# Performance work log

Hardware: AMD Instinct MI355X
Metric: run time of the kernel (lower is better)

The kernel has to match this reference:

```python
import jax, jax.numpy as jnp
import numpy as np

DIM = 512
H = 8
HD = 64          # hidden_dim = dim // num_heads
TD = 64          # time_dim -> time features = 2*TD = 128
LIN = 1536
EPS = 1e-5

def layer_norm(x, g, b):
    mu = jnp.mean(x, axis=-1, keepdims=True)
    var = jnp.mean((x - mu) ** 2, axis=-1, keepdims=True)
    return (x - mu) * jax.lax.rsqrt(var + EPS) * g + b

def setup_inputs() -> dict:
    key = jax.random.key(0)
    ks = jax.random.split(key, 16)
    B, L = 2, 2048
    return {
        "tensor": jax.random.normal(ks[0], (B, L, DIM), jnp.float32),
        "attention_mask": jnp.ones((B, L), jnp.float32),
        "time_angle": jax.random.uniform(ks[1], (H, TD), jnp.float32),
        "head_time_delta": jax.random.uniform(ks[2], (H,), jnp.float32),
        "Qw": jax.random.normal(ks[3], (DIM, H * HD), jnp.float32) * 0.02,
        "q_bias": jnp.zeros((H * HD,), jnp.float32),
        "Kw": jax.random.normal(ks[4], (DIM, H * HD), jnp.float32) * 0.02,
        "Kb": jax.random.normal(ks[5], (H * HD,), jnp.float32) * 0.02,
        "Vw": jax.random.normal(ks[6], (DIM, H * HD), jnp.float32) * 0.02,
        "Vb": jnp.zeros((H * HD,), jnp.float32),
        "Ow": jax.random.normal(ks[7], (H * HD, DIM), jnp.float32) * 0.02,
        "Ob": jnp.zeros((DIM,), jnp.float32),
        "ln1_g": jnp.ones((DIM,), jnp.float32),
        "ln1_b": jnp.zeros((DIM,), jnp.float32),
        "Win": jax.random.normal(ks[8], (DIM, LIN), jnp.float32) * 0.02,
        "b_in": jax.random.normal(ks[9], (LIN,), jnp.float32) * 0.02,
        "Wout": jax.random.normal(ks[10], (LIN, DIM), jnp.float32) * 0.02,
        "b_out": jnp.zeros((DIM,), jnp.float32),
        "ln2_g": jnp.ones((DIM,), jnp.float32),
        "ln2_b": jnp.zeros((DIM,), jnp.float32),
    }

def reference(tensor, attention_mask, time_angle, head_time_delta, Qw, q_bias,
              Kw, Kb, Vw, Vb, Ow, Ob, ln1_g, ln1_b, Win, b_in, Wout, b_out,
              ln2_g, ln2_b):
    B, L = tensor.shape[:2]
    inv_sqrt = 1.0 / np.sqrt(HD).astype(np.float32)
    # queries: sigmoid-gated scalar weight per (b,l,h)
    q = (tensor @ Qw - jnp.exp(q_bias)).reshape(B, L, H, HD)
    q = jax.nn.sigmoid(q) / HD * attention_mask[..., None, None]  # [B,L,H,HD]
    # time features (note: source reuses time_angles for k_time too)
    t = jnp.arange(L, dtype=tensor.dtype)
    ang = (t[:, None, None] + head_time_delta[None, :, None]) * time_angle  # [L,H,TD]
    c, s = jnp.cos(ang), jnp.sin(ang)
    time = jnp.concatenate([c + s, c - s], axis=-1) * inv_sqrt  # [L,H,2TD]
    qt = q.sum(-1)[..., None] * time                            # [B,L,H,2TD]
    # (K branch is dead code in source: computed but never used)
    attn = jnp.einsum('blhd,thd->blth', qt, time)               # [B,L,L,H]
    v = (tensor @ Vw + Vb).reshape(B, L, H, HD)
    comb = jnp.einsum('blth,bthd->blhd', attn, v)               # [B,L,H,HD]
    attn_out = comb.reshape(B, L, H * HD) @ Ow + Ob
    inter = layer_norm(tensor + attn_out, ln1_g, ln1_b)         # dropout = id (eval)
    lin = jax.nn.gelu(inter @ Win + b_in, approximate=True) @ Wout + b_out
    return layer_norm(inter + lin, ln2_g, ln2_b)
```

## Files before the change

### kernel.cpp

```cpp
#include <hip/hip_runtime.h>
#include <hip/hip_bf16.h>

typedef __hip_bfloat16 bf16;
typedef __attribute__((ext_vector_type(8))) __bf16 bf16x8;
typedef __attribute__((ext_vector_type(4))) float f32x4;

#define DIM   512
#define NH    8
#define HDIM  64
#define LIND  1536
#define LSEQ  2048
#define ROWS  4096
#define TF    128
#define KCH   32

__device__ __forceinline__ float b2f(bf16 v){ return __bfloat162float(v); }
__device__ __forceinline__ void stc(float* C, size_t i, float v){ C[i] = v; }
__device__ __forceinline__ void stc(bf16*  C, size_t i, float v){ C[i] = __float2bfloat16(v); }
__device__ __forceinline__ float ldr(const float* p, size_t i){ return p[i]; }
__device__ __forceinline__ float ldr(const bf16*  p, size_t i){ return b2f(p[i]); }

typedef const __attribute__((address_space(1))) unsigned int* gp1_t;
typedef __attribute__((address_space(3))) unsigned int* lp3_t;
__device__ __forceinline__ void gload16(const bf16* g, unsigned short* l) {
    __builtin_amdgcn_global_load_lds((gp1_t)(const void*)g, (lp3_t)(void*)l, 16, 0, 0);
}

__global__ __launch_bounds__(256) void setup_kernel(const float* __restrict__ tensor,
                                                    const float* __restrict__ tang,
                                                    const float* __restrict__ htd,
                                                    const float* __restrict__ Qw,
                                                    const float* __restrict__ Vw,
                                                    const float* __restrict__ Ow,
                                                    const float* __restrict__ Win,
                                                    const float* __restrict__ Wout,
                                                    bf16* __restrict__ tensorb,
                                                    bf16* __restrict__ timef,
                                                    bf16* __restrict__ timefT,
                                                    bf16* __restrict__ QwT,
                                                    bf16* __restrict__ VwT,
                                                    bf16* __restrict__ OwT,
                                                    bf16* __restrict__ WinT,
                                                    bf16* __restrict__ WoutT)
{
    __shared__ unsigned short st0[32][33];
    __shared__ unsigned short st1[32][33];
    __shared__ float t[32][33];

    int id = blockIdx.x;
    if (id < 2048) {
        int i = id * 256 + threadIdx.x;
        float4 v = ((const float4*)tensor)[i];
        bf16 tt[4];
        tt[0] = __float2bfloat16(v.x); tt[1] = __float2bfloat16(v.y);
        tt[2] = __float2bfloat16(v.z); tt[3] = __float2bfloat16(v.w);
        *(uint2*)&tensorb[(size_t)i * 4] = *(uint2*)tt;
        return;
    }
    if (id < 3072) {
        int q = id - 2048;
        int h = q >> 7;
        int dblk = (q >> 6) & 1;
        int lblk = q & 63;
        int d0 = dblk * 32, l0 = lblk * 32;
        int x = threadIdx.x & 31, y = threadIdx.x >> 5;
        float ta = tang[h * 64 + d0 + x];
        float hb = htd[h];
        #pragma unroll
        for (int r = 0; r < 4; ++r) {
            int ll = y + 8 * r;
            float ang = ((float)(l0 + ll) + hb) * ta;
            float s, c;
            sincosf(ang, &s, &c);
            bf16 v0 = __float2bfloat16((c + s) * 0.125f);
            bf16 v1 = __float2bfloat16((c - s) * 0.125f);
            bf16* p = timef + ((size_t)(l0 + ll) * NH + h) * TF;
            p[d0 + x]      = v0;
            p[d0 + x + 64] = v1;
            st0[x][ll] = *(unsigned short*)&v0;
            st1[x][ll] = *(unsigned short*)&v1;
        }
        __syncthreads();
        #pragma unroll
        for (int r = 0; r < 4; ++r) {
            int dd = y + 8 * r;
            unsigned short u0 = st0[dd][x], u1 = st1[dd][x];
            timefT[((size_t)(h * 128 + d0 + dd)) * LSEQ + l0 + x]      = *(bf16*)&u0;
            timefT[((size_t)(h * 128 + d0 + dd + 64)) * LSEQ + l0 + x] = *(bf16*)&u1;
        }
        return;
    }
    id -= 3072;
    const float* in; bf16* out; int R, C, tx, ty;
    if (id < 256)        { in = Qw;   out = QwT;   R = 512;  C = 512;  tx = id & 15; ty = id >> 4; }
    else if (id < 512)   { id -= 256;  in = Vw;   out = VwT;   R = 512;  C = 512;  tx = id & 15; ty = id >> 4; }
    else if (id < 768)   { id -= 512;  in = Ow;   out = OwT;   R = 512;  C = 512;  tx = id & 15; ty = id >> 4; }
    else if (id < 1536)  { id -= 768;  in = Win;  out = WinT;  R = 512;  C = 1536; tx = id % 48; ty = id / 48; }
    else                 { id -= 1536; in = Wout; out = WoutT; R = 1536; C = 512;  tx = id & 15; ty = id >> 4; }

    int bx = tx * 32, by = ty * 32;
    int x = threadIdx.x & 31, y = threadIdx.x >> 5;
    #pragma unroll
    for (int r = 0; r < 32; r += 8)
        t[y + r][x] = in[(size_t)(by + y + r) * C + bx + x];
    __syncthreads();
    #pragma unroll
    for (int r = 0; r < 32; r += 8)
        out[(size_t)(bx + y + r) * R + by + x] = __float2bfloat16(t[x][y + r]);
}

template<int BM, int BN, int EPI, typename OUTT, typename REST>
__global__ __launch_bounds__(256) void gemm_big(const bf16* __restrict__ A,
                                                const bf16* __restrict__ Bt,
                                                const float* __restrict__ bias,
                                                const REST* __restrict__ res,
                                                OUTT* __restrict__ C,
                                                int M, int N, int K)
{
    constexpr int RM = BM / 32, RN = BN / 32;
    constexpr int ITA = BM / 32, ITB = BN / 32;
    __shared__ unsigned short As[2][BM * 64];
    __shared__ unsigned short Bs[2][BN * 64];

    int tid  = threadIdx.x;
    int lane = tid & 63, wave = tid >> 6;
    int wr = wave >> 1, wc = wave & 1;
    int bm = blockIdx.y * BM, bn = blockIdx.x * BN;
    int l15 = lane & 15, lk = lane >> 4;

    const bf16* gA[ITA]; const bf16* gB[ITB];
    #pragma unroll
    for (int it = 0; it < ITA; ++it) {
        int e = it * 256 + tid, row = e >> 3, g = e & 7;
        gA[it] = &A[(size_t)(bm + row) * K + (g ^ (row & 7)) * 8];
    }
    #pragma unroll
    for (int it = 0; it < ITB; ++it) {
        int e = it * 256 + tid, row = e >> 3, g = e & 7;
        gB[it] = &Bt[(size_t)(bn + row) * K + (g ^ (row & 7)) * 8];
    }

    f32x4 acc[RM][RN] = {};
    int NT = K >> 6;

    #pragma unroll
    for (int it = 0; it < ITA; ++it) gload16(gA[it], &As[0][(it * 256 + tid) * 8]);
    #pragma unroll
    for (int it = 0; it < ITB; ++it) gload16(gB[it], &Bs[0][(it * 256 + tid) * 8]);
    __syncthreads();

    for (int t = 0; t < NT; ++t) {
        int cur = t & 1;
        if (t + 1 < NT) {
            #pragma unroll
            for (int it = 0; it < ITA; ++it)
                gload16(gA[it] + (t + 1) * 64, &As[cur ^ 1][(it * 256 + tid) * 8]);
            #pragma unroll
            for (int it = 0; it < ITB; ++it)
                gload16(gB[it] + (t + 1) * 64, &Bs[cur ^ 1][(it * 256 + tid) * 8]);
        }
        #pragma unroll
        for (int s = 0; s < 2; ++s) {
            bf16x8 a[RM], b[RN];
            int g8 = ((s * 4 + lk) ^ (l15 & 7)) * 8;
            #pragma unroll
            for (int m = 0; m < RM; ++m) {
                int row = wr * (BM / 2) + m * 16 + l15;
                a[m] = *(const bf16x8*)&As[cur][row * 64 + g8];
            }
            #pragma unroll
            for (int n = 0; n < RN; ++n) {
                int row = wc * (BN / 2) + n * 16 + l15;
                b[n] = *(const bf16x8*)&Bs[cur][row * 64 + g8];
            }
            #pragma unroll
            for (int m = 0; m < RM; ++m)
                #pragma unroll
                for (int n = 0; n < RN; ++n)
                    acc[m][n] = __builtin_amdgcn_mfma_f32_16x16x32_bf16(a[m], b[n], acc[m][n], 0, 0, 0);
        }
        __syncthreads();
    }

    #pragma unroll
    for (int m = 0; m < RM; ++m) {
        #pragma unroll
        for (int n = 0; n < RN; ++n) {
            int gcol = bn + wc * (BN / 2) + n * 16 + l15;
            float bs = bias[gcol];
            #pragma unroll
            for (int r = 0; r < 4; ++r) {
                int grow = bm + wr * (BM / 2) + m * 16 + lk * 4 + r;
                float x = acc[m][n][r];
                float o;
                if constexpr (EPI == 2) {
                    o = x + bs + ldr(res, (size_t)grow * N + gcol);
                } else if constexpr (EPI == 3) {
                    float t = x + bs;
                    float u = t + 0.044715f * t * t * t;
                    o = 0.5f * t * (1.0f + tanhf(0.7978845608028654f * u));
                } else {
                    o = x + bs + ldr(res, (size_t)grow * N + gcol);
                }
                stc(C, (size_t)grow * N + gcol, o);
            }
        }
    }
}

__global__ __launch_bounds__(256) void gemm_qv(const bf16* __restrict__ A,
                                               const bf16* __restrict__ Bt,
                                               const float* __restrict__ qb,
                                               const float* __restrict__ Vb,
                                               float* __restrict__ qs,
                                               bf16* __restrict__ vT)
{
    constexpr int BM = 64, BN = 128, RM = 2, RN = 4;
    __shared__ unsigned short As[2][BM * 64];
    __shared__ unsigned short Bs[2][BN * 64];
    __shared__ float qsums[2][64];

    const int K = DIM;
    int tid  = threadIdx.x;
    int lane = tid & 63, wave = tid >> 6;
    int wr = wave >> 1, wc = wave & 1;
    int bm = blockIdx.y * BM, bn = blockIdx.x * BN;
    int l15 = lane & 15, lk = lane >> 4;

    const bf16* gA[2]; const bf16* gB[4];
    #pragma unroll
    for (int it = 0; it < 2; ++it) {
        int e = it * 256 + tid, row = e >> 3, g = e & 7;
        gA[it] = &A[(size_t)(bm + row) * K + (g ^ (row & 7)) * 8];
    }
    #pragma unroll
    for (int it = 0; it < 4; ++it) {
        int e = it * 256 + tid, row = e >> 3, g = e & 7;
        gB[it] = &Bt[(size_t)(bn + row) * K + (g ^ (row & 7)) * 8];
    }

    f32x4 acc[RM][RN] = {};
    const int NT = K >> 6;

    #pragma unroll
    for (int it = 0; it < 2; ++it) gload16(gA[it], &As[0][(it * 256 + tid) * 8]);
    #pragma unroll
    for (int it = 0; it < 4; ++it) gload16(gB[it], &Bs[0][(it * 256 + tid) * 8]);
    __syncthreads();

    for (int t = 0; t < NT; ++t) {
        int cur = t & 1;
        if (t + 1 < NT) {
            #pragma unroll
            for (int it = 0; it < 2; ++it)
                gload16(gA[it] + (t + 1) * 64, &As[cur ^ 1][(it * 256 + tid) * 8]);
            #pragma unroll
            for (int it = 0; it < 4; ++it)
                gload16(gB[it] + (t + 1) * 64, &Bs[cur ^ 1][(it * 256 + tid) * 8]);
        }
        #pragma unroll
        for (int s = 0; s < 2; ++s) {
            bf16x8 a[RM], b[RN];
            int g8 = ((s * 4 + lk) ^ (l15 & 7)) * 8;
            #pragma unroll
            for (int m = 0; m < RM; ++m) {
                int row = wr * 32 + m * 16 + l15;
                a[m] = *(const bf16x8*)&As[cur][row * 64 + g8];
            }
            #pragma unroll
            for (int n = 0; n < RN; ++n) {
                int row = wc * 64 + n * 16 + l15;
                b[n] = *(const bf16x8*)&Bs[cur][row * 64 + g8];
            }
            #pragma unroll
            for (int m = 0; m < RM; ++m)
                #pragma unroll
                for (int n = 0; n < RN; ++n)
                    acc[m][n] = __builtin_amdgcn_mfma_f32_16x16x32_bf16(a[m], b[n], acc[m][n], 0, 0, 0);
        }
        __syncthreads();
    }

    if (bn < DIM) {
        float eq[RN];
        #pragma unroll
        for (int n = 0; n < RN; ++n)
            eq[n] = expf(qb[bn + wc * 64 + n * 16 + l15]);
        #pragma unroll
        for (int m = 0; m < RM; ++m) {
            #pragma unroll
            for (int r = 0; r < 4; ++r) {
                float s = 0.f;
                #pragma unroll
                for (int n = 0; n < RN; ++n) {
                    float x = acc[m][n][r] - eq[n];
                    s += 1.0f / (1.0f + expf(-x));
                }
                s *= (1.0f / 64.0f);
                #pragma unroll
                for (int off = 1; off < 16; off <<= 1) s += __shfl_xor(s, off);
                if (l15 == 0)
                    qsums[wc][wr * 32 + m * 16 + lk * 4 + r] = s;
            }
        }
        __syncthreads();
        if (tid < 128) {
            int hh = tid >> 6, row = tid & 63;
            qs[(size_t)(bm + row) * NH + (bn >> 6) + hh] = qsums[hh][row];
        }
    } else {
        unsigned short* tb = &Bs[0][0];
        #pragma unroll
        for (int m = 0; m < RM; ++m) {
            int trow0 = wr * 32 + m * 16 + lk * 4;
            #pragma unroll
            for (int n = 0; n < RN; ++n) {
                int col = wc * 64 + n * 16 + l15;
                float bs = Vb[bn - DIM + col];
                bf16 tmp[4];
                #pragma unroll
                for (int r = 0; r < 4; ++r)
                    tmp[r] = __float2bfloat16(acc[m][n][r] + bs);
                *(uint2*)&tb[col * 72 + trow0] = *(uint2*)tmp;
            }
        }
        __syncthreads();
        #pragma unroll
        for (int rep = 0; rep < 8; ++rep) {
            int idx = rep * 256 + tid;
            int col = idx >> 4;
            int t4  = (idx & 15) * 4;
            uint2 v = *(uint2*)&tb[col * 72 + t4];
            *(uint2*)&vT[(size_t)(bn - DIM + col) * ROWS + bm + t4] = v;
        }
    }
}

__global__ __launch_bounds__(256) void wpart_mfma(const bf16* __restrict__ timefT,
                                                  const bf16* __restrict__ vT,
                                                  float* __restrict__ wpart)
{
    __shared__ unsigned short As[128 * 64];
    __shared__ unsigned short Bs[64 * 64];

    int bh = blockIdx.x;
    int kc = blockIdx.y;
    int b = bh >> 3, h = bh & 7;
    int tid  = threadIdx.x;
    int lane = tid & 63, wave = tid >> 6;
    int wr = wave >> 1, wc = wave & 1;
    int l15 = lane & 15, lk = lane >> 4;
    int k0 = kc * 64;

    const bf16* Abase = timefT + (size_t)h * (128 * LSEQ) + k0;
    const bf16* Bbase = vT + (size_t)h * 64 * ROWS + (size_t)b * LSEQ + k0;

    #pragma unroll
    for (int it = 0; it < 4; ++it) {
        int e = it * 256 + tid, row = e >> 3, g = e & 7;
        gload16(Abase + (size_t)row * LSEQ + (g ^ (row & 7)) * 8, &As[e * 8]);
    }
    #pragma unroll
    for (int it = 0; it < 2; ++it) {
        int e = it * 256 + tid, row = e >> 3, g = e & 7;
        gload16(Bbase + (size_t)row * ROWS + (g ^ (row & 7)) * 8, &Bs[e * 8]);
    }
    __syncthreads();

    f32x4 acc[4][2] = {};
    #pragma unroll
    for (int s = 0; s < 2; ++s) {
        bf16x8 a[4], bv[2];
        int g8 = ((s * 4 + lk) ^ (l15 & 7)) * 8;
        #pragma unroll
        for (int m = 0; m < 4; ++m) {
            int row = wr * 64 + m * 16 + l15;
            a[m] = *(const bf16x8*)&As[row * 64 + g8];
        }
        #pragma unroll
        for (int n = 0; n < 2; ++n) {
            int row = wc * 32 + n * 16 + l15;
            bv[n] = *(const bf16x8*)&Bs[row * 64 + g8];
        }
        #pragma unroll
        for (int m = 0; m < 4; ++m)
            #pragma unroll
            for (int n = 0; n < 2; ++n)
                acc[m][n] = __builtin_amdgcn_mfma_f32_16x16x32_bf16(a[m], bv[n], acc[m][n], 0, 0, 0);
    }

    float* wp = wpart + ((size_t)(kc * 16 + bh)) * (HDIM * TF);
    #pragma unroll
    for (int m = 0; m < 4; ++m) {
        int gd0 = wr * 64 + m * 16 + lk * 4;
        #pragma unroll
        for (int n = 0; n < 2; ++n) {
            int ghd = wc * 32 + n * 16 + l15;
            *(f32x4*)&wp[ghd * TF + gd0] = acc[m][n];
        }
    }
}

__global__ __launch_bounds__(256) void wred_kernel(const float* __restrict__ wpart,
                                                   bf16* __restrict__ WT)
{
    int i = blockIdx.x * 256 + threadIdx.x;
    float s = 0.f;
    #pragma unroll
    for (int kc = 0; kc < KCH; ++kc)
        s += wpart[(size_t)kc * 131072 + i];
    WT[i] = __float2bfloat16(s);
}

__global__ __launch_bounds__(256) void comb_mfma(const bf16* __restrict__ timef,
                                                 const bf16* __restrict__ WT,
                                                 const float* __restrict__ qs,
                                                 const float* __restrict__ mask,
                                                 bf16* __restrict__ comb)
{
    int bh = blockIdx.x;
    int b = bh >> 3, h = bh & 7;
    int lane = threadIdx.x & 63, wave = threadIdx.x >> 6;
    int l15 = lane & 15, lk = lane >> 4;
    int lbase = blockIdx.y * 128 + wave * 32;

    const bf16* wt = WT + (size_t)bh * (HDIM * TF);

    f32x4 acc[2][4] = {};
    #pragma unroll
    for (int ks = 0; ks < 4; ++ks) {
        int kt = ks * 32;
        bf16x8 a[2], bf[4];
        #pragma unroll
        for (int m = 0; m < 2; ++m) {
            int l = lbase + m * 16 + l15;
            a[m] = *(const bf16x8*)&timef[((size_t)l * NH + h) * TF + kt + lk * 8];
        }
        #pragma unroll
        for (int n = 0; n < 4; ++n)
            bf[n] = *(const bf16x8*)&wt[(size_t)(n * 16 + l15) * TF + kt + lk * 8];
        #pragma unroll
        for (int m = 0; m < 2; ++m)
            #pragma unroll
            for (int n = 0; n < 4; ++n)
                acc[m][n] = __builtin_amdgcn_mfma_f32_16x16x32_bf16(a[m], bf[n], acc[m][n], 0, 0, 0);
    }

    #pragma unroll
    for (int m = 0; m < 2; ++m) {
        #pragma unroll
        for (int r = 0; r < 4; ++r) {
            int l = lbase + m * 16 + lk * 4 + r;
            int row = b * LSEQ + l;
            float q = qs[(size_t)row * NH + h] * mask[row];
            #pragma unroll
            for (int n = 0; n < 4; ++n) {
                int hd = n * 16 + l15;
                comb[(size_t)row * DIM + h * HDIM + hd] =
                    __float2bfloat16(q * acc[m][n][r]);
            }
        }
    }
}

template<int OUTBF>
__global__ __launch_bounds__(256) void ln_kernel(const float* __restrict__ X,
                                                 const float* __restrict__ g,
                                                 const float* __restrict__ bta,
                                                 float* __restrict__ outf,
                                                 bf16* __restrict__ outb)
{
    int row = blockIdx.x;
    const float* x = X + (size_t)row * DIM;
    float v0 = x[threadIdx.x], v1 = x[threadIdx.x + 256];
    float s = v0 + v1, s2 = v0 * v0 + v1 * v1;
    #pragma unroll
    for (int off = 1; off < 64; off <<= 1) {
        s  += __shfl_xor(s,  off);
        s2 += __shfl_xor(s2, off);
    }
    __shared__ float sh[2][4];
    int wave = threadIdx.x >> 6, lane = threadIdx.x & 63;
    if (lane == 0) { sh[0][wave] = s; sh[1][wave] = s2; }
    __syncthreads();
    s  = sh[0][0] + sh[0][1] + sh[0][2] + sh[0][3];
    s2 = sh[1][0] + sh[1][1] + sh[1][2] + sh[1][3];
    float mu  = s * (1.0f / DIM);
    float var = s2 * (1.0f / DIM) - mu * mu;
    float inv = rsqrtf(var + 1e-5f);
    int c0 = threadIdx.x, c1 = threadIdx.x + 256;
    float o0 = (v0 - mu) * inv * g[c0] + bta[c0];
    float o1 = (v1 - mu) * inv * g[c1] + bta[c1];
    if constexpr (OUTBF) {
        outb[(size_t)row * DIM + c0] = __float2bfloat16(o0);
        outb[(size_t)row * DIM + c1] = __float2bfloat16(o1);
    } else {
        outf[(size_t)row * DIM + c0] = o0;
        outf[(size_t)row * DIM + c1] = o1;
    }
}

extern "C" void kernel_launch(void* const* d_in, const int* in_sizes, int n_in,
                              void* d_out, int out_size, void* d_ws, size_t ws_size,
                              hipStream_t stream)
{
    const float* tensor = (const float*)d_in[0];
    const float* mask   = (const float*)d_in[1];
    const float* tang   = (const float*)d_in[2];
    const float* htd    = (const float*)d_in[3];
    const float* Qw     = (const float*)d_in[4];
    const float* qb     = (const float*)d_in[5];
    const float* Vw     = (const float*)d_in[8];
    const float* Vb     = (const float*)d_in[9];
    const float* Ow     = (const float*)d_in[10];
    const float* Ob     = (const float*)d_in[11];
    const float* g1     = (const float*)d_in[12];
    const float* b1     = (const float*)d_in[13];
    const float* Win    = (const float*)d_in[14];
    const float* bin    = (const float*)d_in[15];
    const float* Wout   = (const float*)d_in[16];
    const float* bout   = (const float*)d_in[17];
    const float* g2     = (const float*)d_in[18];
    const float* b2     = (const float*)d_in[19];
    float* out = (float*)d_out;

    float* ws = (float*)d_ws;
    bf16*  vT     = (bf16*)(ws + 0);
    bf16*  actb   = (bf16*)(ws + 0);
    bf16*  tensorb= (bf16*)(ws + 1048576);
    bf16*  combb  = tensorb;
    bf16*  timefb = (bf16*)(ws + 2097152);
    bf16*  timefT = (bf16*)(ws + 3145728);
    bf16*  interb = (bf16*)(ws + 3145728);
    float* wpart  = ws + 4194304;
    float* preLN1 = ws + 4194304;
    float* buf5   = ws + 6291456;
    bf16*  WTb    = (bf16*)(ws + 8388608);
    float* qs     = ws + 8454144;
    bf16*  QVwT   = (bf16*)(ws + 8486912);
    bf16*  QwT    = QVwT;
    bf16*  VwT    = QVwT + (size_t)512 * 512;
    bf16*  OwT    = (bf16*)(ws + 8749056);
    bf16*  WinT   = (bf16*)(ws + 8880128);
    bf16*  WoutT  = (bf16*)(ws + 9273344);

    setup_kernel<<<5376, 256, 0, stream>>>(tensor, tang, htd, Qw, Vw, Ow, Win, Wout,
                                           tensorb, timefb, timefT, QwT, VwT, OwT, WinT, WoutT);
    gemm_qv<<<dim3(8, 64), 256, 0, stream>>>(tensorb, QVwT, qb, Vb, qs, vT);
    wpart_mfma<<<dim3(16, KCH), 256, 0, stream>>>(timefT, vT, wpart);
    wred_kernel<<<512, 256, 0, stream>>>(wpart, WTb);
    comb_mfma<<<dim3(16, 16), 256, 0, stream>>>(timefb, WTb, qs, mask, combb);
    gemm_big<64, 64, 2, float, float><<<dim3(8, 64), 256, 0, stream>>>(combb, OwT, Ob, tensor, preLN1, ROWS, DIM, DIM);
    ln_kernel<1><<<ROWS, 256, 0, stream>>>(preLN1, g1, b1, nullptr, interb);
    gemm_big<64, 128, 3, bf16, float><<<dim3(12, 64), 256, 0, stream>>>(interb, WinT, bin, nullptr, actb, ROWS, LIND, DIM);
    gemm_big<64, 64, 4, float, bf16><<<dim3(8, 64), 256, 0, stream>>>(actb, WoutT, bout, interb, buf5, ROWS, DIM, LIND);
    ln_kernel<0><<<ROWS, 256, 0, stream>>>(buf5, g2, b2, out, nullptr);
}
```

Before: 98.78 us.

## Parameterize GEMM K-tile, store partial W sums in bf16, shrink comb tiles

```diff
diff --git a/kernel.cpp b/kernel.cpp
--- a/kernel.cpp
+++ b/kernel.cpp
@@ -109,7 +109,7 @@
         out[(size_t)(bx + y + r) * R + by + x] = __float2bfloat16(t[x][y + r]);
 }
 
-template<int BM, int BN, int EPI, typename OUTT, typename REST>
+template<int BM, int BN, int BK, int EPI, typename OUTT, typename REST>
 __global__ __launch_bounds__(256) void gemm_big(const bf16* __restrict__ A,
                                                 const bf16* __restrict__ Bt,
                                                 const float* __restrict__ bias,
@@ -118,9 +118,10 @@
                                                 int M, int N, int K)
 {
     constexpr int RM = BM / 32, RN = BN / 32;
-    constexpr int ITA = BM / 32, ITB = BN / 32;
-    __shared__ unsigned short As[2][BM * 64];
-    __shared__ unsigned short Bs[2][BN * 64];
+    constexpr int GR = BK / 8;
+    constexpr int ITA = BM * GR / 256, ITB = BN * GR / 256;
+    __shared__ unsigned short As[2][BM * BK];
+    __shared__ unsigned short Bs[2][BN * BK];
 
     int tid  = threadIdx.x;
     int lane = tid & 63, wave = tid >> 6;
@@ -131,17 +132,17 @@
     const bf16* gA[ITA]; const bf16* gB[ITB];
     #pragma unroll
     for (int it = 0; it < ITA; ++it) {
-        int e = it * 256 + tid, row = e >> 3, g = e & 7;
-        gA[it] = &A[(size_t)(bm + row) * K + (g ^ (row & 7)) * 8];
+        int e = it * 256 + tid, row = e / GR, g = e % GR;
+        gA[it] = &A[(size_t)(bm + row) * K + (g ^ (row & (GR - 1))) * 8];
     }
     #pragma unroll
     for (int it = 0; it < ITB; ++it) {
-        int e = it * 256 + tid, row = e >> 3, g = e & 7;
-        gB[it] = &Bt[(size_t)(bn + row) * K + (g ^ (row & 7)) * 8];
+        int e = it * 256 + tid, row = e / GR, g = e % GR;
+        gB[it] = &Bt[(size_t)(bn + row) * K + (g ^ (row & (GR - 1))) * 8];
     }
 
     f32x4 acc[RM][RN] = {};
-    int NT = K >> 6;
+    int NT = K / BK;
 
     #pragma unroll
     for (int it = 0; it < ITA; ++it) gload16(gA[it], &As[0][(it * 256 + tid) * 8]);
@@ -154,24 +155,24 @@
         if (t + 1 < NT) {
             #pragma unroll
             for (int it = 0; it < ITA; ++it)
-                gload16(gA[it] + (t + 1) * 64, &As[cur ^ 1][(it * 256 + tid) * 8]);
+                gload16(gA[it] + (t + 1) * BK, &As[cur ^ 1][(it * 256 + tid) * 8]);
             #pragma unroll
             for (int it = 0; it < ITB; ++it)
-                gload16(gB[it] + (t + 1) * 64, &Bs[cur ^ 1][(it * 256 + tid) * 8]);
-        }
-        #pragma unroll
-        for (int s = 0; s < 2; ++s) {
+                gload16(gB[it] + (t + 1) * BK, &Bs[cur ^ 1][(it * 256 + tid) * 8]);
+        }
+        #pragma unroll
+        for (int s = 0; s < BK / 32; ++s) {
             bf16x8 a[RM], b[RN];
-            int g8 = ((s * 4 + lk) ^ (l15 & 7)) * 8;
+            int g8 = ((s * 4 + lk) ^ (l15 & (GR - 1))) * 8;
             #pragma unroll
             for (int m = 0; m < RM; ++m) {
                 int row = wr * (BM / 2) + m * 16 + l15;
-                a[m] = *(const bf16x8*)&As[cur][row * 64 + g8];
+                a[m] = *(const bf16x8*)&As[cur][row * BK + g8];
             }
             #pragma unroll
             for (int n = 0; n < RN; ++n) {
                 int row = wc * (BN / 2) + n * 16 + l15;
-                b[n] = *(const bf16x8*)&Bs[cur][row * 64 + g8];
+                b[n] = *(const bf16x8*)&Bs[cur][row * BK + g8];
             }
             #pragma unroll
             for (int m = 0; m < RM; ++m)
@@ -338,7 +339,7 @@
 
 __global__ __launch_bounds__(256) void wpart_mfma(const bf16* __restrict__ timefT,
                                                   const bf16* __restrict__ vT,
-                                                  float* __restrict__ wpart)
+                                                  bf16* __restrict__ wpart)
 {
     __shared__ unsigned short As[128 * 64];
     __shared__ unsigned short Bs[64 * 64];
@@ -389,27 +390,37 @@
                 acc[m][n] = __builtin_amdgcn_mfma_f32_16x16x32_bf16(a[m], bv[n], acc[m][n], 0, 0, 0);
     }
 
-    float* wp = wpart + ((size_t)(kc * 16 + bh)) * (HDIM * TF);
+    bf16* wp = wpart + ((size_t)(kc * 16 + bh)) * (HDIM * TF);
     #pragma unroll
     for (int m = 0; m < 4; ++m) {
         int gd0 = wr * 64 + m * 16 + lk * 4;
         #pragma unroll
         for (int n = 0; n < 2; ++n) {
             int ghd = wc * 32 + n * 16 + l15;
-            *(f32x4*)&wp[ghd * TF + gd0] = acc[m][n];
-        }
-    }
-}
-
-__global__ __launch_bounds__(256) void wred_kernel(const float* __restrict__ wpart,
+            bf16 tmp[4];
+            #pragma unroll
+            for (int r = 0; r < 4; ++r) tmp[r] = __float2bfloat16(acc[m][n][r]);
+            *(uint2*)&wp[ghd * TF + gd0] = *(uint2*)tmp;
+        }
+    }
+}
+
+__global__ __launch_bounds__(256) void wred_kernel(const bf16* __restrict__ wpart,
                                                    bf16* __restrict__ WT)
 {
-    int i = blockIdx.x * 256 + threadIdx.x;
-    float s = 0.f;
-    #pragma unroll
-    for (int kc = 0; kc < KCH; ++kc)
-        s += wpart[(size_t)kc * 131072 + i];
-    WT[i] = __float2bfloat16(s);
+    int i4 = (blockIdx.x * 256 + threadIdx.x) * 4;
+    float s[4] = {};
+    #pragma unroll
+    for (int kc = 0; kc < KCH; ++kc) {
+        uint2 u = *(const uint2*)&wpart[(size_t)kc * 131072 + i4];
+        const bf16* p = (const bf16*)&u;
+        #pragma unroll
+        for (int r = 0; r < 4; ++r) s[r] += b2f(p[r]);
+    }
+    bf16 o[4];
+    #pragma unroll
+    for (int r = 0; r < 4; ++r) o[r] = __float2bfloat16(s[r]);
+    *(uint2*)&WT[i4] = *(uint2*)o;
 }
 
 __global__ __launch_bounds__(256) void comb_mfma(const bf16* __restrict__ timef,
@@ -422,43 +433,33 @@
     int b = bh >> 3, h = bh & 7;
     int lane = threadIdx.x & 63, wave = threadIdx.x >> 6;
     int l15 = lane & 15, lk = lane >> 4;
-    int lbase = blockIdx.y * 128 + wave * 32;
+    int lbase = blockIdx.y * 64 + wave * 16;
 
     const bf16* wt = WT + (size_t)bh * (HDIM * TF);
 
-    f32x4 acc[2][4] = {};
+    f32x4 acc[4] = {};
     #pragma unroll
     for (int ks = 0; ks < 4; ++ks) {
         int kt = ks * 32;
-        bf16x8 a[2], bf[4];
-        #pragma unroll
-        for (int m = 0; m < 2; ++m) {
-            int l = lbase + m * 16 + l15;
-            a[m] = *(const bf16x8*)&timef[((size_t)l * NH + h) * TF + kt + lk * 8];
-        }
+        bf16x8 a, bf[4];
+        a = *(const bf16x8*)&timef[((size_t)(lbase + l15) * NH + h) * TF + kt + lk * 8];
         #pragma unroll
         for (int n = 0; n < 4; ++n)
             bf[n] = *(const bf16x8*)&wt[(size_t)(n * 16 + l15) * TF + kt + lk * 8];
         #pragma unroll
-        for (int m = 0; m < 2; ++m)
-            #pragma unroll
-            for (int n = 0; n < 4; ++n)
-                acc[m][n] = __builtin_amdgcn_mfma_f32_16x16x32_bf16(a[m], bf[n], acc[m][n], 0, 0, 0);
-    }
-
-    #pragma unroll
-    for (int m = 0; m < 2; ++m) {
-        #pragma unroll
-        for (int r = 0; r < 4; ++r) {
-            int l = lbase + m * 16 + lk * 4 + r;
-            int row = b * LSEQ + l;
-            float q = qs[(size_t)row * NH + h] * mask[row];
-            #pragma unroll
-            for (int n = 0; n < 4; ++n) {
-                int hd = n * 16 + l15;
-                comb[(size_t)row * DIM + h * HDIM + hd] =
-                    __float2bfloat16(q * acc[m][n][r]);
-            }
+        for (int n = 0; n < 4; ++n)
+            acc[n] = __builtin_amdgcn_mfma_f32_16x16x32_bf16(a, bf[n], acc[n], 0, 0, 0);
+    }
+
+    #pragma unroll
+    for (int r = 0; r < 4; ++r) {
+        int l = lbase + lk * 4 + r;
+        int row = b * LSEQ + l;
+        float q = qs[(size_t)row * NH + h] * mask[row];
+        #pragma unroll
+        for (int n = 0; n < 4; ++n) {
+            int hd = n * 16 + l15;
+            comb[(size_t)row * DIM + h * HDIM + hd] = __float2bfloat16(q * acc[n][r]);
         }
     }
 }
@@ -532,7 +533,7 @@
     bf16*  timefb = (bf16*)(ws + 2097152);
     bf16*  timefT = (bf16*)(ws + 3145728);
     bf16*  interb = (bf16*)(ws + 3145728);
-    float* wpart  = ws + 4194304;
+    bf16*  wpart  = (bf16*)(ws + 4194304);
     float* preLN1 = ws + 4194304;
     float* buf5   = ws + 6291456;
     bf16*  WTb    = (bf16*)(ws + 8388608);
@@ -548,11 +549,11 @@
                                            tensorb, timefb, timefT, QwT, VwT, OwT, WinT, WoutT);
     gemm_qv<<<dim3(8, 64), 256, 0, stream>>>(tensorb, QVwT, qb, Vb, qs, vT);
     wpart_mfma<<<dim3(16, KCH), 256, 0, stream>>>(timefT, vT, wpart);
-    wred_kernel<<<512, 256, 0, stream>>>(wpart, WTb);
-    comb_mfma<<<dim3(16, 16), 256, 0, stream>>>(timefb, WTb, qs, mask, combb);
-    gemm_big<64, 64, 2, float, float><<<dim3(8, 64), 256, 0, stream>>>(combb, OwT, Ob, tensor, preLN1, ROWS, DIM, DIM);
+    wred_kernel<<<128, 256, 0, stream>>>(wpart, WTb);
+    comb_mfma<<<dim3(16, 32), 256, 0, stream>>>(timefb, WTb, qs, mask, combb);
+    gemm_big<64, 64, 128, 2, float, float><<<dim3(8, 64), 256, 0, stream>>>(combb, OwT, Ob, tensor, preLN1, ROWS, DIM, DIM);
     ln_kernel<1><<<ROWS, 256, 0, stream>>>(preLN1, g1, b1, nullptr, interb);
-    gemm_big<64, 128, 3, bf16, float><<<dim3(12, 64), 256, 0, stream>>>(interb, WinT, bin, nullptr, actb, ROWS, LIND, DIM);
-    gemm_big<64, 64, 4, float, bf16><<<dim3(8, 64), 256, 0, stream>>>(actb, WoutT, bout, interb, buf5, ROWS, DIM, LIND);
+    gemm_big<64, 128, 64, 3, bf16, float><<<dim3(12, 64), 256, 0, stream>>>(interb, WinT, bin, nullptr, actb, ROWS, LIND, DIM);
+    gemm_big<64, 64, 128, 4, float, bf16><<<dim3(8, 64), 256, 0, stream>>>(actb, WoutT, bout, interb, buf5, ROWS, DIM, LIND);
     ln_kernel<0><<<ROWS, 256, 0, stream>>>(buf5, g2, b2, out, nullptr);
 }
```

Measured after the change: 97.34 us. Within noise of the previous version (-1.5%).
